# Optimization experiments

Measured on AMD Instinct MI355X. Metric: run time of the kernel, lower is better.

## Reference

```python
import jax, jax.numpy as jnp
from jax import lax
import numpy as np

B, T, D, H, OUT = 2048, 512, 1, 50, 3


def setup_inputs() -> dict:
    key = jax.random.key(0)
    ks = jax.random.split(key, 7)
    s = 1.0 / np.sqrt(H)  # PyTorch LSTM init scale
    x = jax.random.normal(ks[0], (B, T, D), dtype=jnp.float32)
    W_ih = jax.random.uniform(ks[1], (4 * H, D), minval=-s, maxval=s, dtype=jnp.float32)
    W_hh = jax.random.uniform(ks[2], (4 * H, H), minval=-s, maxval=s, dtype=jnp.float32)
    b_ih = jax.random.uniform(ks[3], (4 * H,), minval=-s, maxval=s, dtype=jnp.float32)
    b_hh = jax.random.uniform(ks[4], (4 * H,), minval=-s, maxval=s, dtype=jnp.float32)
    fc_w = jax.random.uniform(ks[5], (OUT, H), minval=-s, maxval=s, dtype=jnp.float32)
    fc_b = jax.random.uniform(ks[6], (OUT,), minval=-s, maxval=s, dtype=jnp.float32)
    return {"x": x, "W_ih": W_ih, "W_hh": W_hh, "b_ih": b_ih, "b_hh": b_hh,
            "fc_w": fc_w, "fc_b": fc_b}


def reference(x, W_ih, W_hh, b_ih, b_hh, fc_w, fc_b):
    # x: [B, T, 1]; PyTorch gate order: i, f, g, o
    b = x.shape[0]
    h = H
    # Precompute input projection for all timesteps: [B, T, 4H]
    x_proj = jnp.einsum('btd,gd->btg', x, W_ih) + b_ih + b_hh

    def step(carry, xp_t):
        h_t, c_t = carry
        gates = xp_t + h_t @ W_hh.T  # [B, 4H]
        i = jax.nn.sigmoid(gates[:, 0 * h:1 * h])
        f = jax.nn.sigmoid(gates[:, 1 * h:2 * h])
        g = jnp.tanh(gates[:, 2 * h:3 * h])
        o = jax.nn.sigmoid(gates[:, 3 * h:4 * h])
        c_new = f * c_t + i * g
        h_new = o * jnp.tanh(c_new)
        return (h_new, c_new), None

    h0 = jnp.zeros((b, h), dtype=x.dtype)
    c0 = jnp.zeros((b, h), dtype=x.dtype)
    (h_T, _), _ = lax.scan(step, (h0, c0), jnp.swapaxes(x_proj, 0, 1))
    # fc on last timestep hidden state only (out[:, -1, :])
    return h_T @ fc_w.T + fc_b
```

## Files before the change

### kernel.cpp

```cpp
#include <hip/hip_runtime.h>


#define BB 2048
#define TT 512
#define HH 50
#define NB 16
#define NW 16
#define XP 513
#define HS 72
#define LO_SCALE  2048.0f
#define LO_ISCALE 0.00048828125f
#define L1 -1.4426950408889634f
#define L2 -2.8853900817779268f

typedef __attribute__((ext_vector_type(4))) float    f32x4;
typedef __attribute__((ext_vector_type(8))) _Float16 f16x8;

__global__ __launch_bounds__(NW * 64)
void lstm_r12_kernel(const float* __restrict__ x,
                     const float* __restrict__ W_ih,
                     const float* __restrict__ W_hh,
                     const float* __restrict__ b_ih,
                     const float* __restrict__ b_hh,
                     const float* __restrict__ fc_w,
                     const float* __restrict__ fc_b,
                     float* __restrict__ out) {
    __shared__ float xs[NB * XP];
    __shared__ __align__(16) unsigned short hf[2][NB][HS];
    __shared__ float hfin[NB][64];

    const int tid  = threadIdx.x;
    const int w    = tid >> 6;
    const int lane = tid & 63;
    const int hi   = lane >> 4;
    const int bcol = lane & 15;
    const int b0   = blockIdx.x * NB;

    for (int idx = tid; idx < NB * TT; idx += NW * 64) {
        xs[(idx >> 9) * XP + (idx & 511)] = x[(b0 + (idx >> 9)) * TT + (idx & 511)];
    }
    if (tid < NB) xs[tid * XP + 512] = 0.0f;
    for (int idx = tid; idx < (int)(sizeof(hf) / 4); idx += NW * 64) {
        ((unsigned*)hf)[idx] = 0;
    }

    const int ga = bcol & 3;
    const int ua = 4 * w + (bcol >> 2);
    const bool ok = (ua < HH);
    const float Lg = (ga == 2) ? L2 : L1;
    f16x8 Ah0, Ah1, Al0, Al1;
    #pragma unroll
    for (int s = 0; s < 2; ++s) {
        #pragma unroll
        for (int e = 0; e < 8; ++e) {
            const int k = 32 * s + 8 * hi + e;
            _Float16 ah = (_Float16)0.0f, al = (_Float16)0.0f;
            if (ok) {
                if (k < HH) {
                    const float wv = Lg * W_hh[(ga * HH + ua) * HH + k];
                    ah = (_Float16)wv;
                    al = (_Float16)((wv - (float)ah) * LO_SCALE);
                } else if (k == 61) {
                    al = (_Float16)(Lg * W_ih[ga * HH + ua]);
                } else if (k == 62) {
                    const float bv = Lg * (b_ih[ga * HH + ua] + b_hh[ga * HH + ua]);
                    ah = (_Float16)bv;
                    al = (_Float16)((bv - (float)ah) * LO_SCALE);
                } else if (k == 63) {
                    const float wv = Lg * W_ih[ga * HH + ua];
                    ah = (_Float16)wv;
                    al = (_Float16)((wv - (float)ah) * LO_SCALE);
                }
            }
            if (s == 0) { Ah0[e] = ah; Al0[e] = al; }
            else        { Ah1[e] = ah; Al1[e] = al; }
        }
    }

    const unsigned short* rb  = &hf[0][bcol][8 * hi];
    unsigned short*       wb  = &hf[0][bcol][4 * w + hi];
    unsigned short*       xwb = &hf[0][bcol][0];
    const bool xwriter = (w == 0) && (hi == 3);
    const bool hwriter = (4 * w + hi) < HH;

    __syncthreads();

    if (xwriter) {
        const unsigned short one_h = __builtin_bit_cast(unsigned short, (_Float16)1.0f);
        xwb[62] = one_h;
        xwb[1152 + 62] = one_h;
        const float x0 = xs[bcol * XP + 0];
        const _Float16 xh = (_Float16)x0;
        const _Float16 xl = (_Float16)((x0 - (float)xh) * LO_SCALE);
        xwb[63] = __builtin_bit_cast(unsigned short, xh);
        xwb[61] = __builtin_bit_cast(unsigned short, xl);
    }

    float c = 0.0f, hcur = 0.0f;
    const f32x4 zero4 = {0.0f, 0.0f, 0.0f, 0.0f};

    __syncthreads();

#define STEP(CB, T) { \
        const f16x8 B0 = *(const f16x8*)(rb + (CB) * 1152); \
        const f16x8 B1 = *(const f16x8*)(rb + (CB) * 1152 + 32); \
        f32x4 acc  = __builtin_amdgcn_mfma_f32_16x16x32_f16(Ah0, B0, zero4, 0, 0, 0); \
        f32x4 acc2 = __builtin_amdgcn_mfma_f32_16x16x32_f16(Al0, B0, zero4, 0, 0, 0); \
        acc  = __builtin_amdgcn_mfma_f32_16x16x32_f16(Ah1, B1, acc,  0, 0, 0); \
        acc2 = __builtin_amdgcn_mfma_f32_16x16x32_f16(Al1, B1, acc2, 0, 0, 0); \
         \
        const float v0 = fmaf(acc2[0], LO_ISCALE, acc[0]); \
        const float v1 = fmaf(acc2[1], LO_ISCALE, acc[1]); \
        const float v2 = fmaf(acc2[2], LO_ISCALE, acc[2]); \
        const float v3 = fmaf(acc2[3], LO_ISCALE, acc[3]); \
        const float E1 = __builtin_amdgcn_exp2f(v0);    \
        const float E2 = __builtin_amdgcn_exp2f(v1);    \
        const float G  = __builtin_amdgcn_exp2f(v2);    \
        const float E4 = __builtin_amdgcn_exp2f(v3);    \
        const float P1 = 1.0f + E1, P2 = 1.0f + E2; \
        const float PG = 1.0f + G,  P4 = 1.0f + E4; \
        const float MG = 1.0f - G; \
        const float N  = fmaf(c * P1, PG, MG * P2); \
        const float D  = (P1 * P2) * PG; \
        c = N * __builtin_amdgcn_rcpf(D); \
        const float C5 = __builtin_amdgcn_exp2f(L2 * c); \
        const float Q  = (1.0f + C5) * P4; \
        hcur = (1.0f - C5) * __builtin_amdgcn_rcpf(Q); \
        if (hwriter) \
            wb[(1 - (CB)) * 1152] = __builtin_bit_cast(unsigned short, (_Float16)hcur); \
        if (xwriter) { \
            const float xn = xs[bcol * XP + (T) + 1]; \
            const _Float16 xh = (_Float16)xn; \
            const _Float16 xl = (_Float16)((xn - (float)xh) * LO_SCALE); \
            xwb[(1 - (CB)) * 1152 + 63] = __builtin_bit_cast(unsigned short, xh); \
            xwb[(1 - (CB)) * 1152 + 61] = __builtin_bit_cast(unsigned short, xl); \
        } \
        __syncthreads(); }

    #pragma unroll 1
    for (int t = 0; t < TT; t += 2) {
        STEP(0, t)
        STEP(1, t + 1)
    }
#undef STEP

    hfin[bcol][4 * w + hi] = hcur;
    __syncthreads();
    if (tid < NB * 3) {
        const int b = tid / 3, o = tid % 3;
        float s = fc_b[o];
        for (int uu = 0; uu < HH; ++uu)
            s = fmaf(hfin[b][uu], fc_w[o * HH + uu], s);
        out[(b0 + b) * 3 + o] = s;
    }
}

extern "C" void kernel_launch(void* const* d_in, const int* in_sizes, int n_in,
                              void* d_out, int out_size, void* d_ws, size_t ws_size,
                              hipStream_t stream) {
    const float* x    = (const float*)d_in[0];
    const float* W_ih = (const float*)d_in[1];
    const float* W_hh = (const float*)d_in[2];
    const float* b_ih = (const float*)d_in[3];
    const float* b_hh = (const float*)d_in[4];
    const float* fc_w = (const float*)d_in[5];
    const float* fc_b = (const float*)d_in[6];
    float* out = (float*)d_out;

    dim3 grid(BB / NB);
    dim3 block(NW * 64);
    lstm_r12_kernel<<<grid, block, 0, stream>>>(x, W_ih, W_hh, b_ih, b_hh,
                                                fc_w, fc_b, out);
}
```

Baseline: 262.8 us.

## Halve waves per block, each wave computes two hidden-unit tiles per step

Cuts the block from 16 to 8 waves. Each wave now holds A fragments for two 4-unit groups and issues 8 MFMAs per step that share the same B loads. The hidden-state buffer is rearranged into a fragment-native 1024-entry layout so each lane reads its B vector contiguously. This is meant to lower per-step barrier cost and redundant LDS reads, at the price of more serial MFMA and gate math per wave and higher register use.

```diff
diff --git a/kernel.cpp b/kernel.cpp
--- a/kernel.cpp
+++ b/kernel.cpp
@@ -5,9 +5,8 @@
 #define TT 512
 #define HH 50
 #define NB 16
-#define NW 16
+#define NW 8
 #define XP 513
-#define HS 72
 #define LO_SCALE  2048.0f
 #define LO_ISCALE 0.00048828125f
 #define L1 -1.4426950408889634f
@@ -16,8 +15,10 @@
 typedef __attribute__((ext_vector_type(4))) float    f32x4;
 typedef __attribute__((ext_vector_type(8))) _Float16 f16x8;
 
+#define F16BITS(v) __builtin_bit_cast(unsigned short, (_Float16)(v))
+
 __global__ __launch_bounds__(NW * 64)
-void lstm_r12_kernel(const float* __restrict__ x,
+void lstm_r13_kernel(const float* __restrict__ x,
                      const float* __restrict__ W_ih,
                      const float* __restrict__ W_hh,
                      const float* __restrict__ b_ih,
@@ -26,7 +27,7 @@
                      const float* __restrict__ fc_b,
                      float* __restrict__ out) {
     __shared__ float xs[NB * XP];
-    __shared__ __align__(16) unsigned short hf[2][NB][HS];
+    __shared__ __align__(16) unsigned short hb[2][1024];
     __shared__ float hfin[NB][64];
 
     const int tid  = threadIdx.x;
@@ -40,79 +41,77 @@
         xs[(idx >> 9) * XP + (idx & 511)] = x[(b0 + (idx >> 9)) * TT + (idx & 511)];
     }
     if (tid < NB) xs[tid * XP + 512] = 0.0f;
-    for (int idx = tid; idx < (int)(sizeof(hf) / 4); idx += NW * 64) {
-        ((unsigned*)hf)[idx] = 0;
+    for (int idx = tid; idx < (int)(sizeof(hb) / 4); idx += NW * 64) {
+        ((unsigned*)hb)[idx] = 0;
     }
 
     const int ga = bcol & 3;
-    const int ua = 4 * w + (bcol >> 2);
-    const bool ok = (ua < HH);
+    const int qa = bcol >> 2;
     const float Lg = (ga == 2) ? L2 : L1;
-    f16x8 Ah0, Ah1, Al0, Al1;
+    f16x8 Ah[2][2], Al[2][2];
     #pragma unroll
-    for (int s = 0; s < 2; ++s) {
+    for (int tt = 0; tt < 2; ++tt) {
+        const int ua = 8 * w + 4 * tt + qa;
+        const bool ok = (ua < HH);
         #pragma unroll
-        for (int e = 0; e < 8; ++e) {
-            const int k = 32 * s + 8 * hi + e;
-            _Float16 ah = (_Float16)0.0f, al = (_Float16)0.0f;
-            if (ok) {
-                if (k < HH) {
-                    const float wv = Lg * W_hh[(ga * HH + ua) * HH + k];
-                    ah = (_Float16)wv;
-                    al = (_Float16)((wv - (float)ah) * LO_SCALE);
-                } else if (k == 61) {
-                    al = (_Float16)(Lg * W_ih[ga * HH + ua]);
-                } else if (k == 62) {
-                    const float bv = Lg * (b_ih[ga * HH + ua] + b_hh[ga * HH + ua]);
-                    ah = (_Float16)bv;
-                    al = (_Float16)((bv - (float)ah) * LO_SCALE);
-                } else if (k == 63) {
-                    const float wv = Lg * W_ih[ga * HH + ua];
-                    ah = (_Float16)wv;
-                    al = (_Float16)((wv - (float)ah) * LO_SCALE);
+        for (int s = 0; s < 2; ++s) {
+            f16x8 vh = {}, vl = {};
+            #pragma unroll
+            for (int e = 0; e < 8; ++e) {
+                const int k = 32 * s + 8 * hi + e;
+                _Float16 ah = (_Float16)0.0f, al = (_Float16)0.0f;
+                if (ok) {
+                    if (k < HH) {
+                        const float wv = Lg * W_hh[(ga * HH + ua) * HH + k];
+                        ah = (_Float16)wv;
+                        al = (_Float16)((wv - (float)ah) * LO_SCALE);
+                    } else if (k == 61) {
+                        al = (_Float16)(Lg * W_ih[ga * HH + ua]);
+                    } else if (k == 62) {
+                        const float bv = Lg * (b_ih[ga * HH + ua] + b_hh[ga * HH + ua]);
+                        ah = (_Float16)bv;
+                        al = (_Float16)((bv - (float)ah) * LO_SCALE);
+                    } else if (k == 63) {
+                        const float wv = Lg * W_ih[ga * HH + ua];
+                        ah = (_Float16)wv;
+                        al = (_Float16)((wv - (float)ah) * LO_SCALE);
+                    }
                 }
+                vh[e] = ah; vl[e] = al;
             }
-            if (s == 0) { Ah0[e] = ah; Al0[e] = al; }
-            else        { Ah1[e] = ah; Al1[e] = al; }
+            Ah[tt][s] = vh; Al[tt][s] = vl;
         }
     }
 
-    const unsigned short* rb  = &hf[0][bcol][8 * hi];
-    unsigned short*       wb  = &hf[0][bcol][4 * w + hi];
-    unsigned short*       xwb = &hf[0][bcol][0];
-    const bool xwriter = (w == 0) && (hi == 3);
-    const bool hwriter = (4 * w + hi) < HH;
+    const unsigned short* rbase = &hb[0][0] + 8 * lane;
+    unsigned short* wb0 = &hb[0][0] + 128 * w + 8 * bcol + hi;
+    const bool hw0 = (8 * w + hi) < HH;
+    const bool hw1 = (8 * w + 4 + hi) < HH;
+    const bool xwriter = (w == 7) && (hi == 3);
+    unsigned short* xwb = &hb[0][0] + 896 + 8 * bcol;
+    const unsigned short one_us = F16BITS(1.0f);
 
     __syncthreads();
 
     if (xwriter) {
-        const unsigned short one_h = __builtin_bit_cast(unsigned short, (_Float16)1.0f);
-        xwb[62] = one_h;
-        xwb[1152 + 62] = one_h;
         const float x0 = xs[bcol * XP + 0];
         const _Float16 xh = (_Float16)x0;
         const _Float16 xl = (_Float16)((x0 - (float)xh) * LO_SCALE);
-        xwb[63] = __builtin_bit_cast(unsigned short, xh);
-        xwb[61] = __builtin_bit_cast(unsigned short, xl);
+        *(unsigned*)(xwb + 6) =
+            (unsigned)one_us | ((unsigned)__builtin_bit_cast(unsigned short, xh) << 16);
+        xwb[5] = __builtin_bit_cast(unsigned short, xl);
     }
 
-    float c = 0.0f, hcur = 0.0f;
+    float c0 = 0.0f, c1 = 0.0f, h0v = 0.0f, h1v = 0.0f;
     const f32x4 zero4 = {0.0f, 0.0f, 0.0f, 0.0f};
 
     __syncthreads();
 
-#define STEP(CB, T) { \
-        const f16x8 B0 = *(const f16x8*)(rb + (CB) * 1152); \
-        const f16x8 B1 = *(const f16x8*)(rb + (CB) * 1152 + 32); \
-        f32x4 acc  = __builtin_amdgcn_mfma_f32_16x16x32_f16(Ah0, B0, zero4, 0, 0, 0); \
-        f32x4 acc2 = __builtin_amdgcn_mfma_f32_16x16x32_f16(Al0, B0, zero4, 0, 0, 0); \
-        acc  = __builtin_amdgcn_mfma_f32_16x16x32_f16(Ah1, B1, acc,  0, 0, 0); \
-        acc2 = __builtin_amdgcn_mfma_f32_16x16x32_f16(Al1, B1, acc2, 0, 0, 0); \
-         \
-        const float v0 = fmaf(acc2[0], LO_ISCALE, acc[0]); \
-        const float v1 = fmaf(acc2[1], LO_ISCALE, acc[1]); \
-        const float v2 = fmaf(acc2[2], LO_ISCALE, acc[2]); \
-        const float v3 = fmaf(acc2[3], LO_ISCALE, acc[3]); \
+#define UPDATE(A, B2, CC, HO) { \
+        const float v0 = fmaf((B2)[0], LO_ISCALE, (A)[0]); \
+        const float v1 = fmaf((B2)[1], LO_ISCALE, (A)[1]); \
+        const float v2 = fmaf((B2)[2], LO_ISCALE, (A)[2]); \
+        const float v3 = fmaf((B2)[3], LO_ISCALE, (A)[3]); \
         const float E1 = __builtin_amdgcn_exp2f(v0);    \
         const float E2 = __builtin_amdgcn_exp2f(v1);    \
         const float G  = __builtin_amdgcn_exp2f(v2);    \
@@ -120,20 +119,35 @@
         const float P1 = 1.0f + E1, P2 = 1.0f + E2; \
         const float PG = 1.0f + G,  P4 = 1.0f + E4; \
         const float MG = 1.0f - G; \
-        const float N  = fmaf(c * P1, PG, MG * P2); \
+        const float N  = fmaf((CC) * P1, PG, MG * P2); \
         const float D  = (P1 * P2) * PG; \
-        c = N * __builtin_amdgcn_rcpf(D); \
-        const float C5 = __builtin_amdgcn_exp2f(L2 * c); \
+        CC = N * __builtin_amdgcn_rcpf(D); \
+        const float C5 = __builtin_amdgcn_exp2f(L2 * (CC)); \
         const float Q  = (1.0f + C5) * P4; \
-        hcur = (1.0f - C5) * __builtin_amdgcn_rcpf(Q); \
-        if (hwriter) \
-            wb[(1 - (CB)) * 1152] = __builtin_bit_cast(unsigned short, (_Float16)hcur); \
+        HO = (1.0f - C5) * __builtin_amdgcn_rcpf(Q); }
+
+#define STEP(CB, T) { \
+        const f16x8 B0 = *(const f16x8*)(rbase + (CB) * 1024); \
+        const f16x8 B1 = *(const f16x8*)(rbase + (CB) * 1024 + 512); \
+        f32x4 p0 = __builtin_amdgcn_mfma_f32_16x16x32_f16(Ah[0][0], B0, zero4, 0, 0, 0); \
+        f32x4 q0 = __builtin_amdgcn_mfma_f32_16x16x32_f16(Al[0][0], B0, zero4, 0, 0, 0); \
+        f32x4 p1 = __builtin_amdgcn_mfma_f32_16x16x32_f16(Ah[1][0], B0, zero4, 0, 0, 0); \
+        f32x4 q1 = __builtin_amdgcn_mfma_f32_16x16x32_f16(Al[1][0], B0, zero4, 0, 0, 0); \
+        p0 = __builtin_amdgcn_mfma_f32_16x16x32_f16(Ah[0][1], B1, p0, 0, 0, 0); \
+        q0 = __builtin_amdgcn_mfma_f32_16x16x32_f16(Al[0][1], B1, q0, 0, 0, 0); \
+        p1 = __builtin_amdgcn_mfma_f32_16x16x32_f16(Ah[1][1], B1, p1, 0, 0, 0); \
+        q1 = __builtin_amdgcn_mfma_f32_16x16x32_f16(Al[1][1], B1, q1, 0, 0, 0); \
+        UPDATE(p0, q0, c0, h0v) \
+        UPDATE(p1, q1, c1, h1v) \
+        if (hw0) wb0[(1 - (CB)) * 1024]     = F16BITS(h0v); \
+        if (hw1) wb0[(1 - (CB)) * 1024 + 4] = F16BITS(h1v); \
         if (xwriter) { \
             const float xn = xs[bcol * XP + (T) + 1]; \
             const _Float16 xh = (_Float16)xn; \
             const _Float16 xl = (_Float16)((xn - (float)xh) * LO_SCALE); \
-            xwb[(1 - (CB)) * 1152 + 63] = __builtin_bit_cast(unsigned short, xh); \
-            xwb[(1 - (CB)) * 1152 + 61] = __builtin_bit_cast(unsigned short, xl); \
+            *(unsigned*)(xwb + (1 - (CB)) * 1024 + 6) = \
+                (unsigned)one_us | ((unsigned)__builtin_bit_cast(unsigned short, xh) << 16); \
+            xwb[(1 - (CB)) * 1024 + 5] = __builtin_bit_cast(unsigned short, xl); \
         } \
         __syncthreads(); }
 
@@ -143,8 +157,10 @@
         STEP(1, t + 1)
     }
 #undef STEP
+#undef UPDATE
 
-    hfin[bcol][4 * w + hi] = hcur;
+    hfin[bcol][8 * w + hi]     = h0v;
+    hfin[bcol][8 * w + 4 + hi] = h1v;
     __syncthreads();
     if (tid < NB * 3) {
         const int b = tid / 3, o = tid % 3;
@@ -169,6 +185,6 @@
 
     dim3 grid(BB / NB);
     dim3 block(NW * 64);
-    lstm_r12_kernel<<<grid, block, 0, stream>>>(x, W_ih, W_hh, b_ih, b_hh,
+    lstm_r13_kernel<<<grid, block, 0, stream>>>(x, W_ih, W_hh, b_ih, b_hh,
                                                 fc_w, fc_b, out);
 }
```

New measurement: 280.0 us. 6.5% more time.
